# Performance work log

Measured on AMD Instinct MI355X. Metric: run time of the kernel, lower is better.

## Reference

```python
import jax, jax.numpy as jnp
import numpy as np


def setup_inputs() -> dict:
    key = jax.random.key(0)
    ks = jax.random.split(key, 5)
    B, S, C = 512, 512, 96
    emissions = jax.random.normal(ks[0], (B, S, C), dtype=jnp.float32)
    tags = jax.random.randint(ks[1], (B, S), 0, C, dtype=jnp.int64)
    masks = jnp.ones((B, S), dtype=bool)
    start_transitions = jax.random.uniform(ks[2], (C,), jnp.float32, -0.1, 0.1)
    end_transitions = jax.random.uniform(ks[3], (C,), jnp.float32, -0.1, 0.1)
    transitions = jax.random.uniform(ks[4], (C, C), jnp.float32, -0.1, 0.1)
    return {
        "emissions": emissions,
        "tags": tags,
        "masks": masks,
        "start_transitions": start_transitions,
        "end_transitions": end_transitions,
        "transitions": transitions,
    }


def _crf_llh(emissions, tags, masks, start_transitions, end_transitions, transitions):
    # to time-major: (S, B, C), (S, B)
    emissions = jnp.swapaxes(emissions, 0, 1)
    tags = jnp.swapaxes(tags, 0, 1)
    masks = jnp.swapaxes(masks, 0, 1)
    S, B, C = emissions.shape
    maskf = masks.astype(emissions.dtype)

    # ---- numerator: score of the gold tag path (fully vectorized over time) ----
    em_scores = jnp.take_along_axis(emissions, tags[:, :, None], axis=2)[:, :, 0]  # (S, B)
    trans_scores = transitions[tags[:-1], tags[1:]]  # (S-1, B)
    score = start_transitions[tags[0]] + em_scores[0]
    score = score + jnp.sum((trans_scores + em_scores[1:]) * maskf[1:], axis=0)
    seq_ends = masks.astype(jnp.int32).sum(axis=0) - 1  # (B,)
    last_tags = tags[seq_ends, jnp.arange(B)]
    numerator = score + end_transitions[last_tags]

    # ---- denominator: forward algorithm (sequential logsumexp recurrence) ----
    alpha0 = start_transitions[None, :] + emissions[0]  # (B, C)

    def step(alpha, inp):
        em_i, m_i = inp  # (B, C), (B,)
        # (B, C_prev, C_next)
        scores = alpha[:, :, None] + transitions[None, :, :] + em_i[:, None, :]
        next_alpha = jax.scipy.special.logsumexp(scores, axis=1)
        alpha = jnp.where(m_i[:, None], next_alpha, alpha)
        return alpha, None

    alpha, _ = jax.lax.scan(step, alpha0, (emissions[1:], masks[1:]))
    denominator = jax.scipy.special.logsumexp(alpha + end_transitions[None, :], axis=1)

    return jnp.mean(numerator - denominator)


def reference(emissions, tags, masks, start_transitions, end_transitions, transitions):
    return _crf_llh(emissions, tags, masks, start_transitions, end_transitions, transitions)
```

## Files before the change

### kernel.cpp

```cpp
#include <hip/hip_runtime.h>
#include <math.h>


#define BATCH 512
#define SEQ   512
#define NC    96
#define NTHR  256
#define CSTR  120
#define GHALF (NC * CSTR)
#define LN2   0.69314718055994531f

typedef __fp16 half2v __attribute__((ext_vector_type(2)));
typedef __fp16 half8  __attribute__((ext_vector_type(8)));
typedef float  f32x4  __attribute__((ext_vector_type(4)));
typedef unsigned int uint2v __attribute__((ext_vector_type(2)));
typedef unsigned int uint4v __attribute__((ext_vector_type(4)));

#define BARRIER() asm volatile("s_waitcnt lgkmcnt(0)\n\ts_barrier" ::: "memory")
#define LGKM0()   asm volatile("s_waitcnt lgkmcnt(0)" ::: "memory")

#define DPP_STEP_F(v, op, ctrl)                                              \
    v = op(v, __int_as_float(__builtin_amdgcn_update_dpp(                    \
            __float_as_int(v), __float_as_int(v), (ctrl), 0xf, 0xf, false)))

__device__ __forceinline__ float fadd_(float a, float b) { return a + b; }
__device__ __forceinline__ float wave_sum_all(float v) {
    DPP_STEP_F(v, fadd_, 0x111);
    DPP_STEP_F(v, fadd_, 0x112);
    DPP_STEP_F(v, fadd_, 0x114);
    DPP_STEP_F(v, fadd_, 0x118);
    DPP_STEP_F(v, fadd_, 0x142);
    DPP_STEP_F(v, fadd_, 0x143);
    return __int_as_float(__builtin_amdgcn_readlane(__float_as_int(v), 63));
}
__device__ __forceinline__ float wave_max_all(float v) {
    DPP_STEP_F(v, fmaxf, 0x111);
    DPP_STEP_F(v, fmaxf, 0x112);
    DPP_STEP_F(v, fmaxf, 0x114);
    DPP_STEP_F(v, fmaxf, 0x118);
    DPP_STEP_F(v, fmaxf, 0x142);
    DPP_STEP_F(v, fmaxf, 0x143);
    return __int_as_float(__builtin_amdgcn_readlane(__float_as_int(v), 63));
}

__device__ __forceinline__ unsigned bcu(half2v h) { return __builtin_bit_cast(unsigned, h); }
__device__ __forceinline__ half2v bch(unsigned u) { return __builtin_bit_cast(half2v, u); }
__device__ __forceinline__ float fdot2_(unsigned a, unsigned b, float c) {
    return __builtin_amdgcn_fdot2(bch(a), bch(b), c, false);
}

__device__ __forceinline__ void matvec96(const __fp16* base, const __fp16* st,
                                         int jj, float& u0, float& u1) {
    const uint4v* c0 = (const uint4v*)(base + (2 * jj) * CSTR);
    const uint4v* c1 = (const uint4v*)(base + (2 * jj) * CSTR + CSTR);
    const uint4v* sp = (const uint4v*)st;
    uint4v g0[12], g1[12], sv[12];
    #pragma unroll
    for (int q = 0; q < 12; ++q) g0[q] = c0[q];
    #pragma unroll
    for (int q = 0; q < 12; ++q) g1[q] = c1[q];
    #pragma unroll
    for (int q = 0; q < 12; ++q) sv[q] = sp[q];
    float a0 = 0.f, a1 = 0.f, a2 = 0.f, a3 = 0.f;
    float b0 = 0.f, b1 = 0.f, b2 = 0.f, b3 = 0.f;
    #pragma unroll
    for (int q = 0; q < 12; ++q) {
        a0 = fdot2_(sv[q].x, g0[q].x, a0);
        a1 = fdot2_(sv[q].y, g0[q].y, a1);
        a2 = fdot2_(sv[q].z, g0[q].z, a2);
        a3 = fdot2_(sv[q].w, g0[q].w, a3);
        b0 = fdot2_(sv[q].x, g1[q].x, b0);
        b1 = fdot2_(sv[q].y, g1[q].y, b1);
        b2 = fdot2_(sv[q].z, g1[q].z, b2);
        b3 = fdot2_(sv[q].w, g1[q].w, b3);
    }
    u0 = (a0 + a1) + (a2 + a3);
    u1 = (b0 + b1) + (b2 + b3);
}

struct PF { float4 a0, a1, b0, b1, c0, c1; };

__device__ __forceinline__ PF ld6(const float* p_base, int row, int g) {
    const float* p = p_base + (size_t)row * NC + 8 * g;
    PF x;
    x.a0 = *(const float4*)(p);      x.a1 = *(const float4*)(p + 4);
    x.b0 = *(const float4*)(p + 32); x.b1 = *(const float4*)(p + 36);
    x.c0 = *(const float4*)(p + 64); x.c1 = *(const float4*)(p + 68);
    return x;
}

__device__ __forceinline__ half8 exp8(float4 u, float4 v) {
    uint4v r;
    r.x = bcu(__builtin_amdgcn_cvt_pkrtz(__expf(u.x), __expf(u.y)));
    r.y = bcu(__builtin_amdgcn_cvt_pkrtz(__expf(u.z), __expf(u.w)));
    r.z = bcu(__builtin_amdgcn_cvt_pkrtz(__expf(v.x), __expf(v.y)));
    r.w = bcu(__builtin_amdgcn_cvt_pkrtz(__expf(v.z), __expf(v.w)));
    return __builtin_bit_cast(half8, r);
}

__global__ __launch_bounds__(NTHR, 2)
void crf_pair_kernel(const float* __restrict__ em,
                     const int*   __restrict__ tags,
                     const int*   __restrict__ masks,
                     const float* __restrict__ startT,
                     const float* __restrict__ endT,
                     const float* __restrict__ trans,
                     float*       __restrict__ out)
{
    const int tid = threadIdx.x;
    const int l   = tid & 63;
    const int w   = tid >> 6;
    const int b   = blockIdx.x;

    __shared__ __align__(16) __fp16 GB[2][GHALF];
    __shared__ __align__(16) __fp16 EB[GHALF];
    __shared__ __align__(16) __fp16 ST[128];

    const float* em_b    = em    + (size_t)b * SEQ * NC;
    const int*   masks_b = masks + (size_t)b * SEQ;

    if (w == 0) {
        const int jj = (l < 48) ? l : (l - 48);

        const float2 st2 = *(const float2*)(startT + 2 * jj);
        const float2 e00 = *(const float2*)(em_b + 2 * jj);
        const float al0 = st2.x + e00.x, al1 = st2.y + e00.y;
        const float M0 = wave_max_all(fmaxf(al0, al1));
        if (l < 48)
            ((unsigned*)ST)[jj] = bcu(__builtin_amdgcn_cvt_pkrtz(
                __expf(al0 - M0), __expf(al1 - M0)));
        int sk = 0;

        float2 e2A = *(const float2*)(em_b + (size_t)2 * NC + 2 * jj);
        float2 e2B = *(const float2*)(em_b + (size_t)4 * NC + 2 * jj);
        int mkA = (masks_b[1] ? 1 : 0) | (masks_b[2] ? 2 : 0);
        int mkB = (masks_b[3] ? 1 : 0) | (masks_b[4] ? 2 : 0);

        auto sstep = [&](int row) {
            LGKM0();
            float v0, v1;
            matvec96(EB, ST, jj, v0, v1);
            const float2 ee = *(const float2*)(em_b + (size_t)row * NC + 2 * jj);
            v0 *= __expf(ee.x); v1 *= __expf(ee.y);
            const float mx = wave_max_all(fmaxf(v0, v1));
            const unsigned ebx = (__float_as_uint(mx) >> 23) & 255u;
            sk += (int)ebx - 127;
            const float sc = __uint_as_float((254u - ebx) << 23);
            if (l < 48)
                ((unsigned*)ST)[jj] = bcu(__builtin_amdgcn_cvt_pkrtz(v0 * sc, v1 * sc));
            LGKM0();
        };

        auto body = [&](int t, float2 e2, int mk) {
            BARRIER();
            float u0, u1;
            matvec96(&GB[t & 1][0], ST, jj, u0, u1);
            if (mk == 3) {
                u0 *= __expf(e2.x); u1 *= __expf(e2.y);
                const float mx = wave_max_all(fmaxf(u0, u1));
                const unsigned ebx = (__float_as_uint(mx) >> 23) & 255u;
                sk += (int)ebx - 127;
                const float sc = __uint_as_float((254u - ebx) << 23);
                if (l < 48)
                    ((unsigned*)ST)[jj] = bcu(__builtin_amdgcn_cvt_pkrtz(u0 * sc, u1 * sc));
            } else {
                if (mk & 1) sstep(2 * t + 1);
                if (mk & 2) sstep(2 * t + 2);
            }
        };

        #pragma unroll 1
        for (int t = 0; t < 254; t += 2) {
            body(t, e2A, mkA);
            {
                const int rb = 2 * t + 6;
                e2A = *(const float2*)(em_b + (size_t)rb * NC + 2 * jj);
                mkA = (masks_b[2 * t + 5] ? 1 : 0) | (masks_b[rb] ? 2 : 0);
            }
            body(t + 1, e2B, mkB);
            {
                const int ra = 2 * t + 7;
                const int rb = (2 * t + 8 > 511) ? 511 : (2 * t + 8);
                e2B = *(const float2*)(em_b + (size_t)rb * NC + 2 * jj);
                mkB = (masks_b[ra] ? 1 : 0) | (masks_b[rb] ? 2 : 0);
            }
        }
        body(254, e2A, mkA);

        LGKM0();
        float u0, u1;
        matvec96(EB, ST, jj, u0, u1);
        const float2 e5 = *(const float2*)(em_b + (size_t)511 * NC + 2 * jj);
        if (masks_b[511]) { u0 *= __expf(e5.x); u1 *= __expf(e5.y); }
        else { u0 = (float)ST[2 * jj]; u1 = (float)ST[2 * jj + 1]; }
        const float2 en = *(const float2*)(endT + 2 * jj);
        const float dvl = (l < 48) ? (u0 * __expf(en.x) + u1 * __expf(en.y)) : 0.f;
        const float dv = wave_sum_all(dvl);
        if (l == 0)
            atomicAdd(out, -(M0 + (float)sk * LN2 + __logf(dv)) * (1.0f / (float)BATCH));
    } else {
        const int lidx = l & 15;
        const int g    = l >> 4;
        const int nt0  = 2 * (w - 1);

        half8 Ea[6][3];
        #pragma unroll
        for (int r = 0; r < 6; ++r)
            #pragma unroll
            for (int c = 0; c < 3; ++c) {
                half8 v;
                #pragma unroll
                for (int e = 0; e < 8; ++e)
                    v[e] = (__fp16)__expf(trans[(16 * r + lidx) * NC + 32 * c + 8 * g + e]);
                Ea[r][c] = v;
            }
        half8 Eb[3][2];
        #pragma unroll
        for (int c = 0; c < 3; ++c)
            #pragma unroll
            for (int ntL = 0; ntL < 2; ++ntL) {
                half8 v;
                #pragma unroll
                for (int e = 0; e < 8; ++e)
                    v[e] = (__fp16)__expf(trans[(32 * c + 8 * g + e) * NC + 16 * (nt0 + ntL) + lidx]);
                Eb[c][ntL] = v;
            }
        #pragma unroll
        for (int ntL = 0; ntL < 2; ++ntL)
            #pragma unroll
            for (int c = 0; c < 3; ++c)
                *(uint4v*)(EB + (16 * (nt0 + ntL) + lidx) * CSTR + 32 * c + 8 * g) =
                    __builtin_bit_cast(uint4v, Eb[c][ntL]);

        auto build = [&](int bsel, const PF& pf) {
            half8 d0 = exp8(pf.a0, pf.a1);
            half8 d1 = exp8(pf.b0, pf.b1);
            half8 d2 = exp8(pf.c0, pf.c1);
            half8 bw[3][2];
            #pragma unroll
            for (int ntL = 0; ntL < 2; ++ntL) {
                bw[0][ntL] = Eb[0][ntL] * d0;
                bw[1][ntL] = Eb[1][ntL] * d1;
                bw[2][ntL] = Eb[2][ntL] * d2;
            }
            __fp16* dst = &GB[bsel][0];
            #pragma unroll
            for (int ntL = 0; ntL < 2; ++ntL) {
                #pragma unroll
                for (int r = 0; r < 6; ++r) {
                    const f32x4 z = {0.f, 0.f, 0.f, 0.f};
                    f32x4 acc = __builtin_amdgcn_mfma_f32_16x16x32_f16(Ea[r][0], bw[0][ntL], z, 0, 0, 0);
                    acc = __builtin_amdgcn_mfma_f32_16x16x32_f16(Ea[r][1], bw[1][ntL], acc, 0, 0, 0);
                    acc = __builtin_amdgcn_mfma_f32_16x16x32_f16(Ea[r][2], bw[2][ntL], acc, 0, 0, 0);
                    uint2v wv;
                    wv.x = bcu(__builtin_amdgcn_cvt_pkrtz(acc[0], acc[1]));
                    wv.y = bcu(__builtin_amdgcn_cvt_pkrtz(acc[2], acc[3]));
                    *(uint2v*)(dst + (16 * (nt0 + ntL) + lidx) * CSTR + 16 * r + 4 * g) = wv;
                }
            }
        };

        {
            const PF p0 = ld6(em_b, 1, g);
            build(0, p0);
        }
        PF r0 = ld6(em_b, 3, g);
        PF r1 = ld6(em_b, 5, g);

        #pragma unroll 1
        for (int t = 0; t < 254; t += 2) {
            BARRIER();
            build(1, r0);
            { const int rr = 2 * t + 7; r0 = ld6(em_b, rr > 511 ? 511 : rr, g); }
            BARRIER();
            build(0, r1);
            { const int rr = 2 * t + 9; r1 = ld6(em_b, rr > 511 ? 511 : rr, g); }
        }
        BARRIER();

        if (w == 1) {
            const int* tb = tags + (size_t)b * SEQ;
            float nsum = 0.f, msum = 0.f;
            #pragma unroll
            for (int kk = 0; kk < 8; ++kk) {
                const int s  = l + 64 * kk;
                const int tg = tb[s];
                const int mk = masks_b[s];
                msum += mk ? 1.f : 0.f;
                if (s == 0) {
                    nsum += startT[tg] + em_b[tg];
                } else if (mk) {
                    nsum += trans[tb[s - 1] * NC + tg] + em_b[(size_t)s * NC + tg];
                }
            }
            nsum = wave_sum_all(nsum);
            msum = wave_sum_all(msum);
            if (l == 0) {
                const int cnt  = (int)msum;
                const int last = tb[cnt - 1];
                atomicAdd(out, (nsum + endT[last]) * (1.0f / (float)BATCH));
            }
        }
    }
}

extern "C" void kernel_launch(void* const* d_in, const int* in_sizes, int n_in,
                              void* d_out, int out_size, void* d_ws, size_t ws_size,
                              hipStream_t stream) {
    const float* em     = (const float*)d_in[0];
    const int*   tags   = (const int*)  d_in[1];
    const int*   masks  = (const int*)  d_in[2];
    const float* startT = (const float*)d_in[3];
    const float* endT   = (const float*)d_in[4];
    const float* trans  = (const float*)d_in[5];
    float* out = (float*)d_out;

    (void)hipMemsetAsync(out, 0, sizeof(float), stream);
    crf_pair_kernel<<<BATCH, NTHR, 0, stream>>>(em, tags, masks, startT, endT, trans, out);
}
```

Baseline: 426.3 us.

## Precompute exp(emissions) to fp16 workspace and re-lay out shared matrices

Adds a separate elementwise kernel that computes exp of all emissions once and stores them as fp16 in the workspace. The main kernel then reads half-size rows for both the builder waves and the recurrence wave, so it no longer issues per-step exp work or fp32 loads. The shared-memory column layout changes from a 120-half stride to 208 bytes with a different split of the columns, and a setprio hint is placed around the recurrence dot product. The cost is an extra launch plus a full write and re-read of a fp16 copy of the emissions; if no workspace is available it falls back to the old in-kernel path.

New measurement: 483.9 us. 1.13x slower.

```diff
diff --git a/kernel.cpp b/kernel.cpp
--- a/kernel.cpp
+++ b/kernel.cpp
@@ -6,8 +6,8 @@
 #define SEQ   512
 #define NC    96
 #define NTHR  256
-#define CSTR  120
-#define GHALF (NC * CSTR)
+#define CBYTES 208
+#define GBYTES (NC * CBYTES)
 #define LN2   0.69314718055994531f
 
 typedef __fp16 half2v __attribute__((ext_vector_type(2)));
@@ -17,7 +17,6 @@
 typedef unsigned int uint4v __attribute__((ext_vector_type(4)));
 
 #define BARRIER() asm volatile("s_waitcnt lgkmcnt(0)\n\ts_barrier" ::: "memory")
-#define LGKM0()   asm volatile("s_waitcnt lgkmcnt(0)" ::: "memory")
 
 #define DPP_STEP_F(v, op, ctrl)                                              \
     v = op(v, __int_as_float(__builtin_amdgcn_update_dpp(                    \
@@ -43,161 +42,199 @@
     return __int_as_float(__builtin_amdgcn_readlane(__float_as_int(v), 63));
 }
 
-__device__ __forceinline__ unsigned bcu(half2v h) { return __builtin_bit_cast(unsigned, h); }
+__device__ __forceinline__ unsigned pk2(float a, float b) {
+    return __builtin_bit_cast(unsigned, __builtin_amdgcn_cvt_pkrtz(a, b));
+}
 __device__ __forceinline__ half2v bch(unsigned u) { return __builtin_bit_cast(half2v, u); }
 __device__ __forceinline__ float fdot2_(unsigned a, unsigned b, float c) {
     return __builtin_amdgcn_fdot2(bch(a), bch(b), c, false);
 }
-
-__device__ __forceinline__ void matvec96(const __fp16* base, const __fp16* st,
-                                         int jj, float& u0, float& u1) {
-    const uint4v* c0 = (const uint4v*)(base + (2 * jj) * CSTR);
-    const uint4v* c1 = (const uint4v*)(base + (2 * jj) * CSTR + CSTR);
-    const uint4v* sp = (const uint4v*)st;
-    uint4v g0[12], g1[12], sv[12];
-    #pragma unroll
-    for (int q = 0; q < 12; ++q) g0[q] = c0[q];
-    #pragma unroll
-    for (int q = 0; q < 12; ++q) g1[q] = c1[q];
-    #pragma unroll
-    for (int q = 0; q < 12; ++q) sv[q] = sp[q];
+__device__ __forceinline__ half8 h8(uint4v u) { return __builtin_bit_cast(half8, u); }
+__device__ __forceinline__ half8 exp8(float4 u, float4 v) {
+    uint4v r;
+    r.x = pk2(__expf(u.x), __expf(u.y));
+    r.y = pk2(__expf(u.z), __expf(u.w));
+    r.z = pk2(__expf(v.x), __expf(v.y));
+    r.w = pk2(__expf(v.z), __expf(v.w));
+    return __builtin_bit_cast(half8, r);
+}
+
+__device__ __forceinline__ void coldot2(const char* colbase, const uint4v* sv,
+                                        float& u0, float& u1) {
     float a0 = 0.f, a1 = 0.f, a2 = 0.f, a3 = 0.f;
     float b0 = 0.f, b1 = 0.f, b2 = 0.f, b3 = 0.f;
     #pragma unroll
     for (int q = 0; q < 12; ++q) {
-        a0 = fdot2_(sv[q].x, g0[q].x, a0);
-        a1 = fdot2_(sv[q].y, g0[q].y, a1);
-        a2 = fdot2_(sv[q].z, g0[q].z, a2);
-        a3 = fdot2_(sv[q].w, g0[q].w, a3);
-        b0 = fdot2_(sv[q].x, g1[q].x, b0);
-        b1 = fdot2_(sv[q].y, g1[q].y, b1);
-        b2 = fdot2_(sv[q].z, g1[q].z, b2);
-        b3 = fdot2_(sv[q].w, g1[q].w, b3);
+        const uint4v x = *(const uint4v*)(colbase + 16 * q);
+        const uint4v y = *(const uint4v*)(colbase + 48 * CBYTES + 16 * q);
+        const uint4v s = sv[q];
+        a0 = fdot2_(s.x, x.x, a0); a1 = fdot2_(s.y, x.y, a1);
+        a2 = fdot2_(s.z, x.z, a2); a3 = fdot2_(s.w, x.w, a3);
+        b0 = fdot2_(s.x, y.x, b0); b1 = fdot2_(s.y, y.y, b1);
+        b2 = fdot2_(s.z, y.z, b2); b3 = fdot2_(s.w, y.w, b3);
     }
     u0 = (a0 + a1) + (a2 + a3);
     u1 = (b0 + b1) + (b2 + b3);
 }
 
-struct PF { float4 a0, a1, b0, b1, c0, c1; };
-
-__device__ __forceinline__ PF ld6(const float* p_base, int row, int g) {
-    const float* p = p_base + (size_t)row * NC + 8 * g;
-    PF x;
-    x.a0 = *(const float4*)(p);      x.a1 = *(const float4*)(p + 4);
-    x.b0 = *(const float4*)(p + 32); x.b1 = *(const float4*)(p + 36);
-    x.c0 = *(const float4*)(p + 64); x.c1 = *(const float4*)(p + 68);
-    return x;
-}
-
-__device__ __forceinline__ half8 exp8(float4 u, float4 v) {
+__global__ __launch_bounds__(256)
+void exp_pre_kernel(const float* __restrict__ em, __fp16* __restrict__ ex) {
+    const size_t i = ((size_t)blockIdx.x * 256 + threadIdx.x) * 8;
+    const float4 a = *(const float4*)(em + i);
+    const float4 b = *(const float4*)(em + i + 4);
     uint4v r;
-    r.x = bcu(__builtin_amdgcn_cvt_pkrtz(__expf(u.x), __expf(u.y)));
-    r.y = bcu(__builtin_amdgcn_cvt_pkrtz(__expf(u.z), __expf(u.w)));
-    r.z = bcu(__builtin_amdgcn_cvt_pkrtz(__expf(v.x), __expf(v.y)));
-    r.w = bcu(__builtin_amdgcn_cvt_pkrtz(__expf(v.z), __expf(v.w)));
-    return __builtin_bit_cast(half8, r);
-}
-
+    r.x = pk2(__expf(a.x), __expf(a.y));
+    r.y = pk2(__expf(a.z), __expf(a.w));
+    r.z = pk2(__expf(b.x), __expf(b.y));
+    r.w = pk2(__expf(b.z), __expf(b.w));
+    *(uint4v*)(ex + i) = r;
+}
+
+template<int UEX>
 __global__ __launch_bounds__(NTHR, 2)
-void crf_pair_kernel(const float* __restrict__ em,
-                     const int*   __restrict__ tags,
-                     const int*   __restrict__ masks,
-                     const float* __restrict__ startT,
-                     const float* __restrict__ endT,
-                     const float* __restrict__ trans,
-                     float*       __restrict__ out)
+void crf_pair2_kernel(const float* __restrict__ em,
+                      const int*   __restrict__ tags,
+                      const int*   __restrict__ masks,
+                      const float* __restrict__ startT,
+                      const float* __restrict__ endT,
+                      const float* __restrict__ trans,
+                      const __fp16* __restrict__ exq,
+                      float*       __restrict__ out)
 {
     const int tid = threadIdx.x;
     const int l   = tid & 63;
     const int w   = tid >> 6;
     const int b   = blockIdx.x;
 
-    __shared__ __align__(16) __fp16 GB[2][GHALF];
-    __shared__ __align__(16) __fp16 EB[GHALF];
-    __shared__ __align__(16) __fp16 ST[128];
-
-    const float* em_b    = em    + (size_t)b * SEQ * NC;
-    const int*   masks_b = masks + (size_t)b * SEQ;
+    __shared__ __align__(16) char  GBm[2][GBYTES];
+    __shared__ __align__(16) char  EBm[GBYTES];
+    __shared__ __align__(16) __fp16 ST[96];
+
+    const float*  em_b    = em    + (size_t)b * SEQ * NC;
+    const int*    masks_b = masks + (size_t)b * SEQ;
+    const __fp16* exq_b   = UEX ? (exq + (size_t)b * SEQ * NC) : (const __fp16*)0;
 
     if (w == 0) {
-        const int jj = (l < 48) ? l : (l - 48);
-
-        const float2 st2 = *(const float2*)(startT + 2 * jj);
-        const float2 e00 = *(const float2*)(em_b + 2 * jj);
-        const float al0 = st2.x + e00.x, al1 = st2.y + e00.y;
-        const float M0 = wave_max_all(fmaxf(al0, al1));
-        if (l < 48)
-            ((unsigned*)ST)[jj] = bcu(__builtin_amdgcn_cvt_pkrtz(
-                __expf(al0 - M0), __expf(al1 - M0)));
+        const bool act = (l < 48);
+
+        float s0 = -1e30f, s1 = -1e30f;
+        if (act) {
+            s0 = startT[l]      + em_b[l];
+            s1 = startT[l + 48] + em_b[l + 48];
+        }
+        const float M0 = wave_max_all(fmaxf(s0, s1));
+        if (act) {
+            ST[l]      = (__fp16)__expf(s0 - M0);
+            ST[l + 48] = (__fp16)__expf(s1 - M0);
+        }
         int sk = 0;
 
-        float2 e2A = *(const float2*)(em_b + (size_t)2 * NC + 2 * jj);
-        float2 e2B = *(const float2*)(em_b + (size_t)4 * NC + 2 * jj);
-        int mkA = (masks_b[1] ? 1 : 0) | (masks_b[2] ? 2 : 0);
-        int mkB = (masks_b[3] ? 1 : 0) | (masks_b[4] ? 2 : 0);
+        auto ldE = [&](int row, float& x0, float& x1) {
+            if (act) {
+                if (UEX) {
+                    x0 = (float)exq_b[(size_t)row * NC + l];
+                    x1 = (float)exq_b[(size_t)row * NC + l + 48];
+                } else {
+                    x0 = __expf(em_b[(size_t)row * NC + l]);
+                    x1 = __expf(em_b[(size_t)row * NC + l + 48]);
+                }
+            } else { x0 = 0.f; x1 = 0.f; }
+        };
 
         auto sstep = [&](int row) {
-            LGKM0();
-            float v0, v1;
-            matvec96(EB, ST, jj, v0, v1);
-            const float2 ee = *(const float2*)(em_b + (size_t)row * NC + 2 * jj);
-            v0 *= __expf(ee.x); v1 *= __expf(ee.y);
+            uint4v sv[12];
+            const uint4v* stp = (const uint4v*)ST;
+            #pragma unroll
+            for (int q = 0; q < 12; ++q) sv[q] = stp[q];
+            float v0 = 0.f, v1 = 0.f;
+            if (act) coldot2((const char*)EBm + l * CBYTES, sv, v0, v1);
+            if (act) {
+                v0 *= __expf(em_b[(size_t)row * NC + l]);
+                v1 *= __expf(em_b[(size_t)row * NC + l + 48]);
+            }
             const float mx = wave_max_all(fmaxf(v0, v1));
             const unsigned ebx = (__float_as_uint(mx) >> 23) & 255u;
             sk += (int)ebx - 127;
             const float sc = __uint_as_float((254u - ebx) << 23);
-            if (l < 48)
-                ((unsigned*)ST)[jj] = bcu(__builtin_amdgcn_cvt_pkrtz(v0 * sc, v1 * sc));
-            LGKM0();
+            if (act) {
+                ST[l]      = (__fp16)(v0 * sc);
+                ST[l + 48] = (__fp16)(v1 * sc);
+            }
         };
 
-        auto body = [&](int t, float2 e2, int mk) {
+        auto body = [&](int t, float e0, float e1, int mk) {
             BARRIER();
-            float u0, u1;
-            matvec96(&GB[t & 1][0], ST, jj, u0, u1);
+            uint4v sv[12];
+            const uint4v* stp = (const uint4v*)ST;
+            #pragma unroll
+            for (int q = 0; q < 12; ++q) sv[q] = stp[q];
+            float u0 = 0.f, u1 = 0.f;
+            __builtin_amdgcn_s_setprio(1);
+            if (act) coldot2((const char*)GBm[t & 1] + l * CBYTES, sv, u0, u1);
+            __builtin_amdgcn_s_setprio(0);
             if (mk == 3) {
-                u0 *= __expf(e2.x); u1 *= __expf(e2.y);
+                u0 *= e0; u1 *= e1;
                 const float mx = wave_max_all(fmaxf(u0, u1));
                 const unsigned ebx = (__float_as_uint(mx) >> 23) & 255u;
                 sk += (int)ebx - 127;
                 const float sc = __uint_as_float((254u - ebx) << 23);
-                if (l < 48)
-                    ((unsigned*)ST)[jj] = bcu(__builtin_amdgcn_cvt_pkrtz(u0 * sc, u1 * sc));
+                if (act) {
+                    ST[l]      = (__fp16)(u0 * sc);
+                    ST[l + 48] = (__fp16)(u1 * sc);
+                }
             } else {
                 if (mk & 1) sstep(2 * t + 1);
                 if (mk & 2) sstep(2 * t + 2);
             }
         };
 
+        float eA0, eA1, eB0, eB1;
+        ldE(2, eA0, eA1);
+        int mkA = (masks_b[1] ? 1 : 0) | (masks_b[2] ? 2 : 0);
+        ldE(4, eB0, eB1);
+        int mkB = (masks_b[3] ? 1 : 0) | (masks_b[4] ? 2 : 0);
+
         #pragma unroll 1
         for (int t = 0; t < 254; t += 2) {
-            body(t, e2A, mkA);
+            body(t, eA0, eA1, mkA);
             {
                 const int rb = 2 * t + 6;
-                e2A = *(const float2*)(em_b + (size_t)rb * NC + 2 * jj);
+                ldE(rb, eA0, eA1);
                 mkA = (masks_b[2 * t + 5] ? 1 : 0) | (masks_b[rb] ? 2 : 0);
             }
-            body(t + 1, e2B, mkB);
+            body(t + 1, eB0, eB1, mkB);
             {
                 const int ra = 2 * t + 7;
                 const int rb = (2 * t + 8 > 511) ? 511 : (2 * t + 8);
-                e2B = *(const float2*)(em_b + (size_t)rb * NC + 2 * jj);
+                ldE(rb, eB0, eB1);
                 mkB = (masks_b[ra] ? 1 : 0) | (masks_b[rb] ? 2 : 0);
             }
         }
-        body(254, e2A, mkA);
-
-        LGKM0();
-        float u0, u1;
-        matvec96(EB, ST, jj, u0, u1);
-        const float2 e5 = *(const float2*)(em_b + (size_t)511 * NC + 2 * jj);
-        if (masks_b[511]) { u0 *= __expf(e5.x); u1 *= __expf(e5.y); }
-        else { u0 = (float)ST[2 * jj]; u1 = (float)ST[2 * jj + 1]; }
-        const float2 en = *(const float2*)(endT + 2 * jj);
-        const float dvl = (l < 48) ? (u0 * __expf(en.x) + u1 * __expf(en.y)) : 0.f;
-        const float dv = wave_sum_all(dvl);
-        if (l == 0)
-            atomicAdd(out, -(M0 + (float)sk * LN2 + __logf(dv)) * (1.0f / (float)BATCH));
+        body(254, eA0, eA1, mkA);
+
+        {
+            uint4v sv[12];
+            const uint4v* stp = (const uint4v*)ST;
+            #pragma unroll
+            for (int q = 0; q < 12; ++q) sv[q] = stp[q];
+            float u0 = 0.f, u1 = 0.f;
+            if (act) coldot2((const char*)EBm + l * CBYTES, sv, u0, u1);
+            float w0 = 0.f, w1 = 0.f;
+            if (act) {
+                if (masks_b[511]) {
+                    u0 *= __expf(em_b[(size_t)511 * NC + l]);
+                    u1 *= __expf(em_b[(size_t)511 * NC + l + 48]);
+                } else {
+                    u0 = (float)ST[l];
+                    u1 = (float)ST[l + 48];
+                }
+                w0 = u0 * __expf(endT[l]);
+                w1 = u1 * __expf(endT[l + 48]);
+            }
+            const float dv = wave_sum_all(w0 + w1);
+            if (l == 0)
+                atomicAdd(out, -(M0 + (float)sk * LN2 + __logf(dv)) * (1.0f / (float)BATCH));
+        }
     } else {
         const int lidx = l & 15;
         const int g    = l >> 4;
@@ -229,13 +266,10 @@
         for (int ntL = 0; ntL < 2; ++ntL)
             #pragma unroll
             for (int c = 0; c < 3; ++c)
-                *(uint4v*)(EB + (16 * (nt0 + ntL) + lidx) * CSTR + 32 * c + 8 * g) =
+                *(uint4v*)(EBm + (16 * (nt0 + ntL) + lidx) * CBYTES + (4 * c + g) * 16) =
                     __builtin_bit_cast(uint4v, Eb[c][ntL]);
 
-        auto build = [&](int bsel, const PF& pf) {
-            half8 d0 = exp8(pf.a0, pf.a1);
-            half8 d1 = exp8(pf.b0, pf.b1);
-            half8 d2 = exp8(pf.c0, pf.c1);
+        auto build = [&](int bsel, half8 d0, half8 d1, half8 d2) {
             half8 bw[3][2];
             #pragma unroll
             for (int ntL = 0; ntL < 2; ++ntL) {
@@ -243,9 +277,11 @@
                 bw[1][ntL] = Eb[1][ntL] * d1;
                 bw[2][ntL] = Eb[2][ntL] * d2;
             }
-            __fp16* dst = &GB[bsel][0];
+            char* dst = GBm[bsel];
             #pragma unroll
             for (int ntL = 0; ntL < 2; ++ntL) {
+                char* cp = dst + (16 * (nt0 + ntL) + lidx) * CBYTES
+                               + 16 * (g >> 1) + 8 * (g & 1);
                 #pragma unroll
                 for (int r = 0; r < 6; ++r) {
                     const f32x4 z = {0.f, 0.f, 0.f, 0.f};
@@ -253,30 +289,65 @@
                     acc = __builtin_amdgcn_mfma_f32_16x16x32_f16(Ea[r][1], bw[1][ntL], acc, 0, 0, 0);
                     acc = __builtin_amdgcn_mfma_f32_16x16x32_f16(Ea[r][2], bw[2][ntL], acc, 0, 0, 0);
                     uint2v wv;
-                    wv.x = bcu(__builtin_amdgcn_cvt_pkrtz(acc[0], acc[1]));
-                    wv.y = bcu(__builtin_amdgcn_cvt_pkrtz(acc[2], acc[3]));
-                    *(uint2v*)(dst + (16 * (nt0 + ntL) + lidx) * CSTR + 16 * r + 4 * g) = wv;
+                    wv.x = pk2(acc[0], acc[1]);
+                    wv.y = pk2(acc[2], acc[3]);
+                    *(uint2v*)(cp + 32 * r) = wv;
                 }
             }
         };
 
-        {
-            const PF p0 = ld6(em_b, 1, g);
-            build(0, p0);
-        }
-        PF r0 = ld6(em_b, 3, g);
-        PF r1 = ld6(em_b, 5, g);
-
-        #pragma unroll 1
-        for (int t = 0; t < 254; t += 2) {
+        if (UEX) {
+            auto ld3 = [&](int row, uint4v& a, uint4v& bq, uint4v& c) {
+                const char* p = (const char*)exq_b + (size_t)row * 192 + 16 * g;
+                a  = *(const uint4v*)(p);
+                bq = *(const uint4v*)(p + 64);
+                c  = *(const uint4v*)(p + 128);
+            };
+            {
+                uint4v a, bq, c;
+                ld3(1, a, bq, c);
+                build(0, h8(a), h8(bq), h8(c));
+            }
+            uint4v p0a, p0b, p0c, p1a, p1b, p1c;
+            ld3(3, p0a, p0b, p0c);
+            ld3(5, p1a, p1b, p1c);
+            #pragma unroll 1
+            for (int t = 0; t < 254; t += 2) {
+                BARRIER();
+                build(1, h8(p0a), h8(p0b), h8(p0c));
+                { const int rr = 2 * t + 7; ld3(rr > 511 ? 511 : rr, p0a, p0b, p0c); }
+                BARRIER();
+                build(0, h8(p1a), h8(p1b), h8(p1c));
+                { const int rr = 2 * t + 9; ld3(rr > 511 ? 511 : rr, p1a, p1b, p1c); }
+            }
             BARRIER();
-            build(1, r0);
-            { const int rr = 2 * t + 7; r0 = ld6(em_b, rr > 511 ? 511 : rr, g); }
+        } else {
+            auto ld6 = [&](int row, float4& x0, float4& x1, float4& x2,
+                           float4& x3, float4& x4, float4& x5) {
+                const float* p = em_b + (size_t)row * NC + 8 * g;
+                x0 = *(const float4*)(p);      x1 = *(const float4*)(p + 4);
+                x2 = *(const float4*)(p + 32); x3 = *(const float4*)(p + 36);
+                x4 = *(const float4*)(p + 64); x5 = *(const float4*)(p + 68);
+            };
+            {
+                float4 x0, x1, x2, x3, x4, x5;
+                ld6(1, x0, x1, x2, x3, x4, x5);
+                build(0, exp8(x0, x1), exp8(x2, x3), exp8(x4, x5));
+            }
+            float4 a0, a1, a2, a3, a4, a5, b0, b1, b2, b3, b4, b5;
+            ld6(3, a0, a1, a2, a3, a4, a5);
+            ld6(5, b0, b1, b2, b3, b4, b5);
+            #pragma unroll 1
+            for (int t = 0; t < 254; t += 2) {
+                BARRIER();
+                build(1, exp8(a0, a1), exp8(a2, a3), exp8(a4, a5));
+                { const int rr = 2 * t + 7; ld6(rr > 511 ? 511 : rr, a0, a1, a2, a3, a4, a5); }
+                BARRIER();
+                build(0, exp8(b0, b1), exp8(b2, b3), exp8(b4, b5));
+                { const int rr = 2 * t + 9; ld6(rr > 511 ? 511 : rr, b0, b1, b2, b3, b4, b5); }
+            }
             BARRIER();
-            build(0, r1);
-            { const int rr = 2 * t + 9; r1 = ld6(em_b, rr > 511 ? 511 : rr, g); }
-        }
-        BARRIER();
+        }
 
         if (w == 1) {
             const int* tb = tags + (size_t)b * SEQ;
@@ -316,5 +387,15 @@
     float* out = (float*)d_out;
 
     (void)hipMemsetAsync(out, 0, sizeof(float), stream);
-    crf_pair_kernel<<<BATCH, NTHR, 0, stream>>>(em, tags, masks, startT, endT, trans, out);
-}
+
+    const size_t exbytes = (size_t)BATCH * SEQ * NC * sizeof(__fp16);
+    if (d_ws != nullptr && ws_size >= exbytes) {
+        const int nelem8 = BATCH * SEQ * NC / 8;
+        exp_pre_kernel<<<nelem8 / 256, 256, 0, stream>>>(em, (__fp16*)d_ws);
+        crf_pair2_kernel<1><<<BATCH, NTHR, 0, stream>>>(
+            em, tags, masks, startT, endT, trans, (const __fp16*)d_ws, out);
+    } else {
+        crf_pair2_kernel<0><<<BATCH, NTHR, 0, stream>>>(
+            em, tags, masks, startT, endT, trans, (const __fp16*)0, out);
+    }
+}
```
